# Kernel optimization log

Hardware: AMD Instinct MI355X
Metric: run time of the kernel (lower is better)

Reference implementation:

```python
import jax, jax.numpy as jnp
import numpy as np

WIN = (4, 4, 4)   # (wd, wh, ww), window seq len s = 64
HEADS = 4


def setup_inputs() -> dict:
    key = jax.random.key(0)
    k1, k2, k3 = jax.random.split(key, 3)
    B, D, H, W, C = 1, 32, 64, 128, 96
    x = jax.random.normal(k1, (B, D, H, W, C), dtype=jnp.float32)
    # weights stored in (in, out) layout; math identical to torch Linear (x @ W.T)
    w_qkv = jax.random.normal(k2, (C, 3 * C), dtype=jnp.float32) * (C ** -0.5)
    w_proj = jax.random.normal(k3, (C, C), dtype=jnp.float32) * (C ** -0.5)
    b_proj = jnp.zeros((C,), dtype=jnp.float32)
    return {"x": x, "w_qkv": w_qkv, "w_proj": w_proj, "b_proj": b_proj}


def reference(x, w_qkv, w_proj, b_proj):
    B, D, H, W, C = x.shape
    wd, wh, ww = WIN
    h = HEADS
    ch = C // h
    s = wd * wh * ww
    scale = ch ** -0.5
    n, m, l = D // wd, H // wh, W // ww
    # window partition: [B,D,H,W,C] -> [B,n,m,l,s,C]
    xw = x.reshape(B, n, wd, m, wh, l, ww, C)
    xw = xw.transpose(0, 1, 3, 5, 2, 4, 6, 7).reshape(B, n, m, l, s, C)
    # QKV projection (no bias)
    qkv = xw @ w_qkv                      # [B,n,m,l,s,3C]
    q, k, v = jnp.split(qkv, 3, axis=-1)  # each [B,n,m,l,s,C]

    def to_heads(t):
        return t.reshape(B, n, m, l, s, h, ch).transpose(0, 1, 2, 3, 5, 4, 6)

    q, k, v = to_heads(q), to_heads(k), to_heads(v)  # [B,n,m,l,h,s,ch]
    attn = jnp.einsum('bnmlhsc,bnmlhtc->bnmlhst', q, k) * scale
    attn = jax.nn.softmax(attn, axis=-1)             # [B,n,m,l,h,s,s]
    out = jnp.einsum('bnmlhst,bnmlhtc->bnmlhsc', attn, v)
    # merge heads: [B,n,m,l,h,s,ch] -> [B,n,m,l,s,C]
    out = out.transpose(0, 1, 2, 3, 5, 4, 6).reshape(B, n, m, l, s, C)
    out = out @ w_proj + b_proj
    # window merge back to [B,D,H,W,C]
    out = out.reshape(B, n, m, l, wd, wh, ww, C)
    out = out.transpose(0, 1, 4, 2, 5, 3, 6, 7).reshape(B, D, H, W, C)
    return out
```

## Files before the change

### kernel.cpp

```cpp
#include <hip/hip_runtime.h>
#include <hip/hip_bf16.h>

typedef __attribute__((ext_vector_type(8))) short bf16x8;
typedef __attribute__((ext_vector_type(4))) float f32x4;
typedef __attribute__((ext_vector_type(4))) unsigned short u16x4;
typedef __attribute__((ext_vector_type(4))) unsigned int u32x4;
typedef __attribute__((ext_vector_type(2))) unsigned int u32x2;

#define MFMA16(a, b, c) __builtin_amdgcn_mfma_f32_16x16x32_bf16((a), (b), (c), 0, 0, 0)

#define WQT_ELEMS 27648
#define WPT_ELEMS 9216

__device__ __forceinline__ unsigned short cvt_bf(float f) {
    __hip_bfloat16 h = __float2bfloat16(f);
    return *reinterpret_cast<unsigned short*>(&h);
}
__device__ __forceinline__ unsigned pack2bf(float a, float b) {
    return (unsigned)cvt_bf(a) | ((unsigned)cvt_bf(b) << 16);
}

__global__ void wconv_kernel(const float* __restrict__ wqkv,
                             const float* __restrict__ wproj,
                             unsigned short* __restrict__ wsT) {
    int o = blockIdx.x * 256 + threadIdx.x;
    if (o < WQT_ELEMS) {
        int j = o / 96, c = o % 96;
        float w = wqkv[c * 288 + j];
        if (j < 96) w *= 0.2944889313f;
        wsT[o] = cvt_bf(w);
    } else if (o < WQT_ELEMS + WPT_ELEMS) {
        int o2 = o - WQT_ELEMS;
        int j = o2 / 96, c = o2 % 96;
        wsT[o] = cvt_bf(wproj[c * 96 + j]);
    }
}

__device__ __forceinline__ int xq_addr(int t, int c) {
    return ((c >> 5) << 12) + ((t >> 1) << 7)
         + ((((t & 1) << 6) + ((c & 31) << 1)) ^ (((t >> 1) & 7) << 4));
}

__global__ __launch_bounds__(256, 4)
void winattn_kernel(const float* __restrict__ x,
                    const unsigned short* __restrict__ wsT,
                    const float* __restrict__ bproj,
                    float* __restrict__ out) {
    __shared__ __align__(16) char LDS[40960];
    char* xq  = LDS;
    char* ksb = LDS + 12288;
    char* vtb = LDS + 28672;
    float* fbuf = reinterpret_cast<float*>(LDS + 12288);

    const int tid = threadIdx.x;
    const int lane = tid & 63;
    const int wv = tid >> 6;
    const int p  = lane & 15;
    const int qg = lane >> 4;

    const int iw  = blockIdx.x;
    const int l_i = iw & 31;
    const int m_i = (iw >> 5) & 15;
    const int n_i = iw >> 9;

    const f32x4 fzero = {0.f, 0.f, 0.f, 0.f};

    const int ntile = (wv < 2) ? 5 : 4;
    const int tbase = (wv < 2) ? wv * 5 : 10 + (wv - 2) * 4;

    bf16x8 bpre[3];
    #pragma unroll
    for (int kt = 0; kt < 3; ++kt)
        bpre[kt] = *reinterpret_cast<const bf16x8*>(&wsT[(tbase * 16 + p) * 96 + kt * 32 + qg * 8]);

    #pragma unroll
    for (int it = 0; it < 6; ++it) {
        int slot = tid + it * 256;
        int t = slot / 24, cq = slot % 24;
        int td = t >> 4, th = (t >> 2) & 3, tw = t & 3;
        int off = (((n_i * 4 + td) * 64 + (m_i * 4 + th)) * 128 + (l_i * 4 + tw)) * 96 + cq * 4;
        float4 v4 = *reinterpret_cast<const float4*>(x + off);
        u16x4 h;
        h[0] = cvt_bf(v4.x); h[1] = cvt_bf(v4.y); h[2] = cvt_bf(v4.z); h[3] = cvt_bf(v4.w);
        *reinterpret_cast<u16x4*>(xq + xq_addr(t, cq * 4)) = h;
    }
    {
        int t = tid >> 2, hd = tid & 3;
        bf16x8 z = {0, 0, 0, 0, 0, 0, 0, 0};
        int cb = hd * 64 + 48;
        *reinterpret_cast<bf16x8*>(ksb + t * 256 + (cb ^ ((t & 7) << 4))) = z;
    }
    __syncthreads();

    bf16x8 afr[4][3];
    #pragma unroll
    for (int nt = 0; nt < 4; ++nt)
        #pragma unroll
        for (int kt = 0; kt < 3; ++kt)
            afr[nt][kt] = *reinterpret_cast<const bf16x8*>(xq + xq_addr(nt * 16 + p, kt * 32 + qg * 8));
    __syncthreads();

    #pragma unroll
    for (int i = 0; i < 5; ++i) {
        if (i >= ntile) break;
        int m = tbase + i;
        bf16x8 wcur[3] = {bpre[0], bpre[1], bpre[2]};
        if (i + 1 < ntile) {
            #pragma unroll
            for (int kt = 0; kt < 3; ++kt)
                bpre[kt] = *reinterpret_cast<const bf16x8*>(&wsT[((m + 1) * 16 + p) * 96 + kt * 32 + qg * 8]);
        }
        f32x4 acc[4] = {fzero, fzero, fzero, fzero};
        #pragma unroll
        for (int kt = 0; kt < 3; ++kt)
            #pragma unroll
            for (int nt = 0; nt < 4; ++nt)
                acc[nt] = MFMA16(wcur[kt], afr[nt][kt], acc[nt]);
        if (m < 6) {
            int ch = m * 16 + 4 * qg;
            #pragma unroll
            for (int nt = 0; nt < 4; ++nt) {
                u32x2 w = { pack2bf(acc[nt][0], acc[nt][1]), pack2bf(acc[nt][2], acc[nt][3]) };
                *reinterpret_cast<u32x2*>(xq + xq_addr(nt * 16 + p, ch)) = w;
            }
        } else if (m < 12) {
            int jk = (m - 6) * 16 + 4 * qg;
            int cb = jk * 2 + (jk / 24) * 16;
            #pragma unroll
            for (int nt = 0; nt < 4; ++nt) {
                int t = nt * 16 + p;
                u32x2 w = { pack2bf(acc[nt][0], acc[nt][1]), pack2bf(acc[nt][2], acc[nt][3]) };
                *reinterpret_cast<u32x2*>(ksb + t * 256 + (cb ^ ((t & 7) << 4))) = w;
            }
        } else {
            int jv = (m - 12) * 16 + 4 * qg;
            #pragma unroll
            for (int nt = 0; nt < 4; ++nt) {
                int t2 = (nt * 16 + p) * 2;
                #pragma unroll
                for (int rg = 0; rg < 4; ++rg) {
                    int row = jv + rg;
                    *reinterpret_cast<unsigned short*>(vtb + row * 128 + (t2 ^ ((row & 7) << 4))) = cvt_bf(acc[nt][rg]);
                }
            }
        }
    }
    __syncthreads();

    #pragma unroll 1
    for (int hd = 0; hd < 4; ++hd) {
        bf16x8 aqh = *reinterpret_cast<const bf16x8*>(xq + xq_addr(wv * 16 + p, hd * 24 + qg * 8));
        f32x4 sacc[4];
        #pragma unroll
        for (int nt = 0; nt < 4; ++nt) {
            int t = nt * 16 + p;
            bf16x8 ak = *reinterpret_cast<const bf16x8*>(ksb + t * 256 + ((hd * 64 + qg * 16) ^ ((t & 7) << 4)));
            sacc[nt] = MFMA16(ak, aqh, fzero);
        }
        float mm = sacc[0][0];
        #pragma unroll
        for (int nt = 0; nt < 4; ++nt)
            #pragma unroll
            for (int rg = 0; rg < 4; ++rg)
                mm = fmaxf(mm, sacc[nt][rg]);
        mm = fmaxf(mm, __shfl_xor(mm, 16));
        mm = fmaxf(mm, __shfl_xor(mm, 32));
        float pw[4][4];
        float sum = 0.f;
        #pragma unroll
        for (int nt = 0; nt < 4; ++nt)
            #pragma unroll
            for (int rg = 0; rg < 4; ++rg) {
                float e = exp2f(sacc[nt][rg] - mm);
                pw[nt][rg] = e;
                sum += e;
            }
        sum += __shfl_xor(sum, 16);
        sum += __shfl_xor(sum, 32);
        float inv = 1.0f / sum;
        unsigned pk[4][2];
        #pragma unroll
        for (int nt = 0; nt < 4; ++nt) {
            pk[nt][0] = pack2bf(pw[nt][0] * inv, pw[nt][1] * inv);
            pk[nt][1] = pack2bf(pw[nt][2] * inv, pw[nt][3] * inv);
        }
        u32x4 pa0, pa1;
        #pragma unroll
        for (int d = 0; d < 4; ++d) {
            int src = ((qg & 1) * 2 + (d >> 1)) * 16 + p;
            int lo0 = __shfl((int)pk[0][d & 1], src);
            int hi0 = __shfl((int)pk[1][d & 1], src);
            int lo1 = __shfl((int)pk[2][d & 1], src);
            int hi1 = __shfl((int)pk[3][d & 1], src);
            pa0[d] = (qg < 2) ? (unsigned)lo0 : (unsigned)hi0;
            pa1[d] = (qg < 2) ? (unsigned)lo1 : (unsigned)hi1;
        }
        bf16x8 a0 = __builtin_bit_cast(bf16x8, pa0);
        bf16x8 a1 = __builtin_bit_cast(bf16x8, pa1);
        f32x4 oacc[2] = {fzero, fzero};
        #pragma unroll
        for (int n2 = 0; n2 < 2; ++n2) {
            int vr = hd * 24 + n2 * 16 + p;
            vr = vr > 95 ? 95 : vr;
            int rb = vr * 128, sw = (vr & 7) << 4;
            bf16x8 av0 = *reinterpret_cast<const bf16x8*>(vtb + rb + ((qg * 16) ^ sw));
            bf16x8 av1 = *reinterpret_cast<const bf16x8*>(vtb + rb + ((64 + qg * 16) ^ sw));
            oacc[n2] = MFMA16(av0, a0, oacc[n2]);
            oacc[n2] = MFMA16(av1, a1, oacc[n2]);
        }
        {
            u32x2 w0 = { pack2bf(oacc[0][0], oacc[0][1]), pack2bf(oacc[0][2], oacc[0][3]) };
            *reinterpret_cast<u32x2*>(xq + xq_addr(wv * 16 + p, hd * 24 + 4 * qg)) = w0;
            if (qg < 2) {
                u32x2 w1 = { pack2bf(oacc[1][0], oacc[1][1]), pack2bf(oacc[1][2], oacc[1][3]) };
                *reinterpret_cast<u32x2*>(xq + xq_addr(wv * 16 + p, hd * 24 + 16 + 4 * qg)) = w1;
            }
        }
    }

    bf16x8 ofr[3];
    #pragma unroll
    for (int kt = 0; kt < 3; ++kt)
        ofr[kt] = *reinterpret_cast<const bf16x8*>(xq + xq_addr(wv * 16 + p, kt * 32 + qg * 8));
    __syncthreads();

    const unsigned short* wpT = wsT + WQT_ELEMS;
    bf16x8 wpre[3];
    #pragma unroll
    for (int kt = 0; kt < 3; ++kt)
        wpre[kt] = *reinterpret_cast<const bf16x8*>(&wpT[p * 96 + kt * 32 + qg * 8]);
    #pragma unroll
    for (int m = 0; m < 6; ++m) {
        bf16x8 wcur[3] = {wpre[0], wpre[1], wpre[2]};
        if (m < 5) {
            #pragma unroll
            for (int kt = 0; kt < 3; ++kt)
                wpre[kt] = *reinterpret_cast<const bf16x8*>(&wpT[((m + 1) * 16 + p) * 96 + kt * 32 + qg * 8]);
        }
        f32x4 acc = fzero;
        #pragma unroll
        for (int kt = 0; kt < 3; ++kt)
            acc = MFMA16(wcur[kt], ofr[kt], acc);
        float4 bb = *reinterpret_cast<const float4*>(bproj + m * 16 + 4 * qg);
        f32x4 r;
        r[0] = acc[0] + bb.x; r[1] = acc[1] + bb.y;
        r[2] = acc[2] + bb.z; r[3] = acc[3] + bb.w;
        *reinterpret_cast<f32x4*>(fbuf + (wv * 16 + p) * 100 + m * 16 + 4 * qg) = r;
    }
    __syncthreads();

    #pragma unroll
    for (int it = 0; it < 6; ++it) {
        int slot = tid + it * 256;
        int t = slot / 24, cq = slot % 24;
        int td = t >> 4, th = (t >> 2) & 3, tw = t & 3;
        int off = (((n_i * 4 + td) * 64 + (m_i * 4 + th)) * 128 + (l_i * 4 + tw)) * 96 + cq * 4;
        float4 v4 = *reinterpret_cast<const float4*>(fbuf + t * 100 + cq * 4);
        *reinterpret_cast<float4*>(out + off) = v4;
    }
}

extern "C" void kernel_launch(void* const* d_in, const int* in_sizes, int n_in,
                              void* d_out, int out_size, void* d_ws, size_t ws_size,
                              hipStream_t stream) {
    const float* x     = (const float*)d_in[0];
    const float* wqkv  = (const float*)d_in[1];
    const float* wproj = (const float*)d_in[2];
    const float* bproj = (const float*)d_in[3];
    float* out = (float*)d_out;
    unsigned short* wsT = (unsigned short*)d_ws;

    wconv_kernel<<<dim3((WQT_ELEMS + WPT_ELEMS) / 256), dim3(256), 0, stream>>>(wqkv, wproj, wsT);
    winattn_kernel<<<dim3(4096), dim3(256), 0, stream>>>(x, wsT, bproj, out);
}
```

Before: 84.49 us.

## Split QKV projection into token halves with separate Q buffer to cut registers

Gives Q its own LDS buffer instead of overwriting the bf16 input, which removes the barrier between reading the input fragments and writing Q. The QKV projection now runs in two passes over 32-token halves, so only half the A fragments stay in registers. Weight loads are software-pipelined with explicit per-wave schedules. LDS grows from 40 KB to 52 KB and launch bounds drop to 3 blocks per CU, trading occupancy for lower register pressure and one fewer barrier. Weight fragments are now loaded twice, once per half.

```diff
diff --git a/kernel.cpp b/kernel.cpp
--- a/kernel.cpp
+++ b/kernel.cpp
@@ -41,16 +41,18 @@
          + ((((t & 1) << 6) + ((c & 31) << 1)) ^ (((t >> 1) & 7) << 4));
 }
 
-__global__ __launch_bounds__(256, 4)
+__global__ __launch_bounds__(256, 3)
 void winattn_kernel(const float* __restrict__ x,
                     const unsigned short* __restrict__ wsT,
                     const float* __restrict__ bproj,
                     float* __restrict__ out) {
-    __shared__ __align__(16) char LDS[40960];
-    char* xq  = LDS;
-    char* ksb = LDS + 12288;
-    char* vtb = LDS + 28672;
-    float* fbuf = reinterpret_cast<float*>(LDS + 12288);
+    __shared__ __align__(16) char XQ[12288];
+    __shared__ __align__(16) char QK[28672];
+    __shared__ __align__(16) char VT[12288];
+    char* qb  = QK;
+    char* ksb = QK + 12288;
+    char* vtb = VT;
+    float* fbuf = reinterpret_cast<float*>(QK);
 
     const int tid = threadIdx.x;
     const int lane = tid & 63;
@@ -64,14 +66,6 @@
     const int n_i = iw >> 9;
 
     const f32x4 fzero = {0.f, 0.f, 0.f, 0.f};
-
-    const int ntile = (wv < 2) ? 5 : 4;
-    const int tbase = (wv < 2) ? wv * 5 : 10 + (wv - 2) * 4;
-
-    bf16x8 bpre[3];
-    #pragma unroll
-    for (int kt = 0; kt < 3; ++kt)
-        bpre[kt] = *reinterpret_cast<const bf16x8*>(&wsT[(tbase * 16 + p) * 96 + kt * 32 + qg * 8]);
 
     #pragma unroll
     for (int it = 0; it < 6; ++it) {
@@ -82,7 +76,7 @@
         float4 v4 = *reinterpret_cast<const float4*>(x + off);
         u16x4 h;
         h[0] = cvt_bf(v4.x); h[1] = cvt_bf(v4.y); h[2] = cvt_bf(v4.z); h[3] = cvt_bf(v4.w);
-        *reinterpret_cast<u16x4*>(xq + xq_addr(t, cq * 4)) = h;
+        *reinterpret_cast<u16x4*>(XQ + xq_addr(t, cq * 4)) = h;
     }
     {
         int t = tid >> 2, hd = tid & 3;
@@ -92,64 +86,104 @@
     }
     __syncthreads();
 
-    bf16x8 afr[4][3];
-    #pragma unroll
-    for (int nt = 0; nt < 4; ++nt)
+    auto load_w = [&](int m, bf16x8* wc) {
         #pragma unroll
         for (int kt = 0; kt < 3; ++kt)
-            afr[nt][kt] = *reinterpret_cast<const bf16x8*>(xq + xq_addr(nt * 16 + p, kt * 32 + qg * 8));
-    __syncthreads();
-
-    #pragma unroll
-    for (int i = 0; i < 5; ++i) {
-        if (i >= ntile) break;
-        int m = tbase + i;
-        bf16x8 wcur[3] = {bpre[0], bpre[1], bpre[2]};
-        if (i + 1 < ntile) {
-            #pragma unroll
-            for (int kt = 0; kt < 3; ++kt)
-                bpre[kt] = *reinterpret_cast<const bf16x8*>(&wsT[((m + 1) * 16 + p) * 96 + kt * 32 + qg * 8]);
-        }
-        f32x4 acc[4] = {fzero, fzero, fzero, fzero};
-        #pragma unroll
-        for (int kt = 0; kt < 3; ++kt)
-            #pragma unroll
-            for (int nt = 0; nt < 4; ++nt)
-                acc[nt] = MFMA16(wcur[kt], afr[nt][kt], acc[nt]);
-        if (m < 6) {
+            wc[kt] = *reinterpret_cast<const bf16x8*>(&wsT[(m * 16 + p) * 96 + kt * 32 + qg * 8]);
+    };
+
+    #pragma unroll
+    for (int h = 0; h < 2; ++h) {
+        bf16x8 a2[2][3];
+        #pragma unroll
+        for (int j = 0; j < 2; ++j)
+            #pragma unroll
+            for (int kt = 0; kt < 3; ++kt)
+                a2[j][kt] = *reinterpret_cast<const bf16x8*>(XQ + xq_addr((h * 2 + j) * 16 + p, kt * 32 + qg * 8));
+
+        auto doQ = [&](int m, const bf16x8* wc) {
+            f32x4 acc[2] = {fzero, fzero};
+            #pragma unroll
+            for (int kt = 0; kt < 3; ++kt)
+                #pragma unroll
+                for (int j = 0; j < 2; ++j)
+                    acc[j] = MFMA16(wc[kt], a2[j][kt], acc[j]);
             int ch = m * 16 + 4 * qg;
             #pragma unroll
-            for (int nt = 0; nt < 4; ++nt) {
-                u32x2 w = { pack2bf(acc[nt][0], acc[nt][1]), pack2bf(acc[nt][2], acc[nt][3]) };
-                *reinterpret_cast<u32x2*>(xq + xq_addr(nt * 16 + p, ch)) = w;
-            }
-        } else if (m < 12) {
+            for (int j = 0; j < 2; ++j) {
+                u32x2 w = { pack2bf(acc[j][0], acc[j][1]), pack2bf(acc[j][2], acc[j][3]) };
+                *reinterpret_cast<u32x2*>(qb + xq_addr((h * 2 + j) * 16 + p, ch)) = w;
+            }
+        };
+        auto doK = [&](int m, const bf16x8* wc) {
+            f32x4 acc[2] = {fzero, fzero};
+            #pragma unroll
+            for (int kt = 0; kt < 3; ++kt)
+                #pragma unroll
+                for (int j = 0; j < 2; ++j)
+                    acc[j] = MFMA16(wc[kt], a2[j][kt], acc[j]);
             int jk = (m - 6) * 16 + 4 * qg;
             int cb = jk * 2 + (jk / 24) * 16;
             #pragma unroll
-            for (int nt = 0; nt < 4; ++nt) {
-                int t = nt * 16 + p;
-                u32x2 w = { pack2bf(acc[nt][0], acc[nt][1]), pack2bf(acc[nt][2], acc[nt][3]) };
+            for (int j = 0; j < 2; ++j) {
+                int t = (h * 2 + j) * 16 + p;
+                u32x2 w = { pack2bf(acc[j][0], acc[j][1]), pack2bf(acc[j][2], acc[j][3]) };
                 *reinterpret_cast<u32x2*>(ksb + t * 256 + (cb ^ ((t & 7) << 4))) = w;
             }
-        } else {
+        };
+        auto doV = [&](int m, const bf16x8* wc) {
+            f32x4 acc[2] = {fzero, fzero};
+            #pragma unroll
+            for (int kt = 0; kt < 3; ++kt)
+                #pragma unroll
+                for (int j = 0; j < 2; ++j)
+                    acc[j] = MFMA16(wc[kt], a2[j][kt], acc[j]);
             int jv = (m - 12) * 16 + 4 * qg;
             #pragma unroll
-            for (int nt = 0; nt < 4; ++nt) {
-                int t2 = (nt * 16 + p) * 2;
+            for (int j = 0; j < 2; ++j) {
+                int t2 = ((h * 2 + j) * 16 + p) * 2;
                 #pragma unroll
                 for (int rg = 0; rg < 4; ++rg) {
                     int row = jv + rg;
-                    *reinterpret_cast<unsigned short*>(vtb + row * 128 + (t2 ^ ((row & 7) << 4))) = cvt_bf(acc[nt][rg]);
+                    *reinterpret_cast<unsigned short*>(vtb + row * 128 + (t2 ^ ((row & 7) << 4))) = cvt_bf(acc[j][rg]);
                 }
             }
+        };
+
+        bf16x8 wA[3], wB[3];
+        if (wv == 0) {
+            load_w(0, wA);
+            load_w(1, wB); doQ(0, wA);
+            load_w(2, wA); doQ(1, wB);
+            load_w(3, wB); doQ(2, wA);
+            load_w(4, wA); doQ(3, wB);
+            doQ(4, wA);
+        } else if (wv == 1) {
+            load_w(5, wA);
+            load_w(6, wB); doQ(5, wA);
+            load_w(7, wA); doK(6, wB);
+            load_w(8, wB); doK(7, wA);
+            load_w(9, wA); doK(8, wB);
+            doK(9, wA);
+        } else if (wv == 2) {
+            load_w(10, wA);
+            load_w(11, wB); doK(10, wA);
+            load_w(12, wA); doK(11, wB);
+            load_w(13, wB); doV(12, wA);
+            doV(13, wB);
+        } else {
+            load_w(14, wA);
+            load_w(15, wB); doV(14, wA);
+            load_w(16, wA); doV(15, wB);
+            load_w(17, wB); doV(16, wA);
+            doV(17, wB);
         }
     }
     __syncthreads();
 
     #pragma unroll 1
     for (int hd = 0; hd < 4; ++hd) {
-        bf16x8 aqh = *reinterpret_cast<const bf16x8*>(xq + xq_addr(wv * 16 + p, hd * 24 + qg * 8));
+        bf16x8 aqh = *reinterpret_cast<const bf16x8*>(qb + xq_addr(wv * 16 + p, hd * 24 + qg * 8));
         f32x4 sacc[4];
         #pragma unroll
         for (int nt = 0; nt < 4; ++nt) {
@@ -210,10 +244,10 @@
         }
         {
             u32x2 w0 = { pack2bf(oacc[0][0], oacc[0][1]), pack2bf(oacc[0][2], oacc[0][3]) };
-            *reinterpret_cast<u32x2*>(xq + xq_addr(wv * 16 + p, hd * 24 + 4 * qg)) = w0;
+            *reinterpret_cast<u32x2*>(XQ + xq_addr(wv * 16 + p, hd * 24 + 4 * qg)) = w0;
             if (qg < 2) {
                 u32x2 w1 = { pack2bf(oacc[1][0], oacc[1][1]), pack2bf(oacc[1][2], oacc[1][3]) };
-                *reinterpret_cast<u32x2*>(xq + xq_addr(wv * 16 + p, hd * 24 + 16 + 4 * qg)) = w1;
+                *reinterpret_cast<u32x2*>(XQ + xq_addr(wv * 16 + p, hd * 24 + 16 + 4 * qg)) = w1;
             }
         }
     }
@@ -221,7 +255,7 @@
     bf16x8 ofr[3];
     #pragma unroll
     for (int kt = 0; kt < 3; ++kt)
-        ofr[kt] = *reinterpret_cast<const bf16x8*>(xq + xq_addr(wv * 16 + p, kt * 32 + qg * 8));
+        ofr[kt] = *reinterpret_cast<const bf16x8*>(XQ + xq_addr(wv * 16 + p, kt * 32 + qg * 8));
     __syncthreads();
 
     const unsigned short* wpT = wsT + WQT_ELEMS;
```

Result: slower. 204.7 us (+142.3%).
